# Optimization experiments

Measured on AMD Instinct MI355X. Metric: run time of the kernel, lower is better.

The kernel has to match this reference:

```python
import jax, jax.numpy as jnp
import numpy as np

NEG_INF = -1e9


def setup_inputs() -> dict:
    key = jax.random.key(0)
    ks = jax.random.split(key, 6)
    B, S, E, D = 32, 2048, 1024, 1024
    dec_hidden = jax.random.normal(ks[0], (B, D), dtype=jnp.float32)
    enc_outputs = jax.random.normal(ks[1], (B, S, E), dtype=jnp.float32)
    mask = jax.random.randint(ks[2], (B, S), 0, 2, dtype=jnp.int32)
    # scale weights ~ Glorot-ish so tanh isn't saturated
    W_enc = jax.random.normal(ks[3], (D, E), dtype=jnp.float32) / np.sqrt(E)
    W_dec = jax.random.normal(ks[4], (D, D), dtype=jnp.float32) / np.sqrt(D)
    v = jax.random.normal(ks[5], (D,), dtype=jnp.float32) / np.sqrt(D)
    return {"dec_hidden": dec_hidden, "enc_outputs": enc_outputs, "mask": mask,
            "W_enc": W_enc, "W_dec": W_dec, "v": v}


def reference(dec_hidden, enc_outputs, mask, W_enc, W_dec, v):
    # dh: [B, D]  (torch Linear: x @ W.T)
    dh = dec_hidden @ W_dec.T
    # eh: [B, S, D]
    eh = jnp.einsum('bse,de->bsd', enc_outputs, W_enc)
    # additive energy + projection by v -> scores [B, S]
    energy = jnp.tanh(dh[:, None, :] + eh)
    scores = jnp.einsum('bsd,d->bs', energy, v)
    scores = jnp.where(mask == 0, NEG_INF, scores)
    weights = jax.nn.softmax(scores, axis=1)          # [B, S]
    context = jnp.einsum('bs,bse->be', weights, enc_outputs)  # [B, E]
    return context, weights
```

## Files before the change

### kernel.cpp

```cpp
#include <hip/hip_runtime.h>
#include <stdint.h>

typedef float f32x4 __attribute__((ext_vector_type(4)));
typedef float f32x16 __attribute__((ext_vector_type(16)));
typedef short bf16x8 __attribute__((ext_vector_type(8)));
typedef unsigned short ushort8 __attribute__((ext_vector_type(8)));

__device__ __forceinline__ unsigned short f2bf(float x) {
  union { float f; uint32_t u; } c; c.f = x;
  return (unsigned short)((c.u + 0x8000u) >> 16);
}
__device__ __forceinline__ float bf2f(unsigned short u) {
  union { uint32_t u; float f; } c; c.u = ((uint32_t)u) << 16;
  return c.f;
}


__global__ void prep_fused_k(const float* __restrict__ W, unsigned short* __restrict__ Wt,
                             const float* __restrict__ dec, const float* __restrict__ Wd,
                             float* __restrict__ dh) {
  if (blockIdx.x < 512) {
    int t = blockIdx.x * 256 + threadIdx.x;
    int d  = t >> 7;
    int c0 = (t & 127) << 3;
    const float* src = W + ((size_t)d << 10) + c0;
    f32x4 f0 = *(const f32x4*)src;
    f32x4 f1 = *(const f32x4*)(src + 4);
    ushort8 u;
    u[0]=f2bf(f0[0]); u[1]=f2bf(f0[1]); u[2]=f2bf(f0[2]); u[3]=f2bf(f0[3]);
    u[4]=f2bf(f1[0]); u[5]=f2bf(f1[1]); u[6]=f2bf(f1[2]); u[7]=f2bf(f1[3]);
    int nt = d >> 7, r = d & 127;
    int kt = c0 >> 5, kb = (c0 & 31) >> 3;
    *(ushort8*)(Wt + (((size_t)(nt * 32 + kt)) << 12) + kb * 1024 + r * 8) = u;
  } else {
    __shared__ float sdec[1024];
    int bb = blockIdx.x - 512;
    int b = bb >> 2;
    for (int i = threadIdx.x; i < 1024; i += 256) sdec[i] = dec[(b << 10) + i];
    __syncthreads();
    int d = ((bb & 3) << 8) + threadIdx.x;
    const float* wr = Wd + ((size_t)d << 10);
    float a = 0.f;
    for (int k = 0; k < 1024; k += 4) {
      f32x4 wv = *(const f32x4*)(wr + k);
      f32x4 xv = *(const f32x4*)(&sdec[k]);
      a += wv[0]*xv[0] + wv[1]*xv[1] + wv[2]*xv[2] + wv[3]*xv[3];
    }
    dh[(b << 10) + d] = a;
  }
}

__global__ void compact_k(const int* __restrict__ mask, int* __restrict__ rows,
                          int* __restrict__ cnt, float* __restrict__ wout) {
  int b = blockIdx.x, tid = threadIdx.x;
  int lane = tid & 63, wv = tid >> 6;
  int mloc[8]; int c = 0;
  #pragma unroll
  for (int ii = 0; ii < 8; ++ii) {
    int s = tid * 8 + ii;
    int m = mask[(b << 11) + s];
    mloc[ii] = m; c += m;
    wout[(b << 11) + s] = 0.f;
  }
  int inc = c;
  #pragma unroll
  for (int off = 1; off < 64; off <<= 1) {
    int nn = __shfl_up(inc, off);
    if (lane >= off) inc += nn;
  }
  __shared__ int wsum[4];
  if (lane == 63) wsum[wv] = inc;
  __syncthreads();
  int base = 0;
  for (int w = 0; w < wv; ++w) base += wsum[w];
  int idx = base + inc - c;
  #pragma unroll
  for (int ii = 0; ii < 8; ++ii) {
    if (mloc[ii]) { rows[(b << 11) + idx] = tid * 8 + ii; ++idx; }
  }
  if (tid == 0) cnt[b] = wsum[0] + wsum[1] + wsum[2] + wsum[3];
}

__global__ void pack7_k(const float* __restrict__ enc, const int* __restrict__ rows,
                        const int* __restrict__ cnt, unsigned short* __restrict__ encP) {
  int b = blockIdx.x >> 4, mt = blockIdx.x & 15;
  int n = cnt[b];
  if (mt * 128 >= n) return;
  __shared__ int sr[128];
  if (threadIdx.x < 128) {
    int i = mt * 128 + threadIdx.x; if (i >= n) i = n - 1;
    sr[threadIdx.x] = rows[(b << 11) + i];
  }
  __syncthreads();
  unsigned short* dst = encP + (((size_t)(b * 16 + mt)) << 17);
  for (int it = 0; it < 64; ++it) {
    int idx = it * 256 + threadIdx.x;
    int r   = idx >> 7;
    int c0  = (idx & 127) << 3;
    const float* src = enc + (((size_t)(b << 11) + sr[r]) << 10) + c0;
    f32x4 f0 = *(const f32x4*)src;
    f32x4 f1 = *(const f32x4*)(src + 4);
    ushort8 u;
    u[0]=f2bf(f0[0]); u[1]=f2bf(f0[1]); u[2]=f2bf(f0[2]); u[3]=f2bf(f0[3]);
    u[4]=f2bf(f1[0]); u[5]=f2bf(f1[1]); u[6]=f2bf(f1[2]); u[7]=f2bf(f1[3]);
    int kt = c0 >> 5, kb = (c0 & 31) >> 3;
    *(ushort8*)(dst + (kt << 12) + kb * 1024 + r * 8) = u;
  }
}

__global__ __launch_bounds__(256, 3) void score7_k(
    const unsigned short* __restrict__ encP, const unsigned short* __restrict__ Wt,
    const float* __restrict__ dh, const float* __restrict__ v,
    const int* __restrict__ cnt, float* __restrict__ pscores)
{
  int L  = (blockIdx.x & 7) * 512 + (blockIdx.x >> 3);
  int b  = L >> 7, mt = (L >> 3) & 15, nt = L & 7;
  int n  = cnt[b];
  if (mt * 128 >= n) return;

  __shared__ __align__(16) unsigned short AS[2][4096];
  __shared__ __align__(16) unsigned short BS[2][4096];
  __shared__ float sc[128][2];

  int tid  = threadIdx.x;
  int lane = tid & 63;
  int wv   = tid >> 6;
  int wm = wv >> 1, wn = wv & 1;
  int l31 = lane & 31, l5 = lane >> 5;

  const unsigned short* aT = encP + (((size_t)(b * 16 + mt)) << 17);
  const unsigned short* bT = Wt + (((size_t)nt) << 17);

  int offA[2][2], offB[2][2];
  #pragma unroll
  for (int mf = 0; mf < 2; ++mf) {
    int r = wm * 64 + mf * 32 + l31;
    #pragma unroll
    for (int ki = 0; ki < 2; ++ki)
      offA[mf][ki] = ((ki * 2 + l5) << 10) + r * 8;
  }
  #pragma unroll
  for (int nf = 0; nf < 2; ++nf) {
    int r = wn * 64 + nf * 32 + l31;
    #pragma unroll
    for (int ki = 0; ki < 2; ++ki)
      offB[nf][ki] = ((ki * 2 + l5) << 10) + r * 8;
  }

  f32x16 acc[2][2];
  #pragma unroll
  for (int i = 0; i < 2; ++i)
    #pragma unroll
    for (int j = 0; j < 2; ++j)
      #pragma unroll
      for (int e = 0; e < 16; ++e)
        acc[i][j][e] = 0.f;

  auto stage = [&](int slot, int kt) {
    #pragma unroll
    for (int j = 0; j < 2; ++j) {
      int chunk = wv * 2 + j;
      __builtin_amdgcn_global_load_lds(
        (const __attribute__((address_space(1))) void*)(const void*)(aT + ((size_t)kt << 12) + chunk * 512 + lane * 8),
        (__attribute__((address_space(3))) void*)(void*)(&AS[slot][chunk * 512]), 16, 0, 0);
      __builtin_amdgcn_global_load_lds(
        (const __attribute__((address_space(1))) void*)(const void*)(bT + ((size_t)kt << 12) + chunk * 512 + lane * 8),
        (__attribute__((address_space(3))) void*)(void*)(&BS[slot][chunk * 512]), 16, 0, 0);
    }
  };

  auto compute = [&](int slot) {
    bf16x8 af[2][2], bf[2][2];
    #pragma unroll
    for (int mf = 0; mf < 2; ++mf)
      #pragma unroll
      for (int ki = 0; ki < 2; ++ki)
        af[mf][ki] = *(const bf16x8*)&AS[slot][offA[mf][ki]];
    #pragma unroll
    for (int nf = 0; nf < 2; ++nf)
      #pragma unroll
      for (int ki = 0; ki < 2; ++ki)
        bf[nf][ki] = *(const bf16x8*)&BS[slot][offB[nf][ki]];
    #pragma unroll
    for (int ki = 0; ki < 2; ++ki)
      #pragma unroll
      for (int mf = 0; mf < 2; ++mf)
        #pragma unroll
        for (int nf = 0; nf < 2; ++nf)
          acc[mf][nf] = __builtin_amdgcn_mfma_f32_32x32x16_bf16(af[mf][ki], bf[nf][ki], acc[mf][nf], 0, 0, 0);
  };

  stage(0, 0);
  __syncthreads();
  int slot = 0;
  for (int kt = 0; kt < 31; ++kt) {
    stage(slot ^ 1, kt + 1);
    compute(slot);
    __syncthreads();
    slot ^= 1;
  }
  compute(slot);

  float vv[2], dd[2];
  #pragma unroll
  for (int nf = 0; nf < 2; ++nf) {
    int dcol = nt * 128 + wn * 64 + nf * 32 + l31;
    vv[nf] = v[dcol];
    dd[nf] = dh[(b << 10) + dcol];
  }
  #pragma unroll
  for (int mf = 0; mf < 2; ++mf) {
    #pragma unroll
    for (int reg = 0; reg < 16; ++reg) {
      float p = 0.f;
      #pragma unroll
      for (int nf = 0; nf < 2; ++nf) {
        float x = acc[mf][nf][reg] + dd[nf];
        float e = __expf(2.0f * x);
        float t = 1.0f - __fdividef(2.0f, e + 1.0f);
        p += vv[nf] * t;
      }
      p += __shfl_xor(p, 1); p += __shfl_xor(p, 2); p += __shfl_xor(p, 4);
      p += __shfl_xor(p, 8); p += __shfl_xor(p, 16);
      if (l31 == 0) {
        int row = wm * 64 + mf * 32 + (reg & 3) + 8 * (reg >> 2) + 4 * l5;
        sc[row][wn] = p;
      }
    }
  }
  __syncthreads();
  if (tid < 128) {
    int i = mt * 128 + tid;
    if (i < n)
      pscores[(((size_t)nt) << 16) + (b << 11) + i] = sc[tid][0] + sc[tid][1];
  }
}

__global__ void softmax4_k(const float* __restrict__ ps, const int* __restrict__ rows,
                           const int* __restrict__ cnt, float* __restrict__ wout,
                           float* __restrict__ wc) {
  int b = blockIdx.x;
  int tid = threadIdx.x;
  int n = cnt[b];
  float val[8];
  float m = -INFINITY;
  #pragma unroll
  for (int ii = 0; ii < 8; ++ii) {
    int i = tid + ii * 256;
    float s = -INFINITY;
    if (i < n) {
      s = 0.f;
      #pragma unroll
      for (int nt = 0; nt < 8; ++nt) s += ps[(((size_t)nt) << 16) + (b << 11) + i];
    }
    val[ii] = s;
    m = fmaxf(m, s);
  }
  #pragma unroll
  for (int off = 1; off < 64; off <<= 1) m = fmaxf(m, __shfl_xor(m, off));
  __shared__ float r1[4], r2[4];
  if ((tid & 63) == 0) r1[tid >> 6] = m;
  __syncthreads();
  m = fmaxf(fmaxf(r1[0], r1[1]), fmaxf(r1[2], r1[3]));
  float ssum = 0.f;
  #pragma unroll
  for (int ii = 0; ii < 8; ++ii) { val[ii] = __expf(val[ii] - m); ssum += val[ii]; }
  #pragma unroll
  for (int off = 1; off < 64; off <<= 1) ssum += __shfl_xor(ssum, off);
  if ((tid & 63) == 0) r2[tid >> 6] = ssum;
  __syncthreads();
  ssum = r2[0] + r2[1] + r2[2] + r2[3];
  float inv = 1.0f / ssum;
  #pragma unroll
  for (int ii = 0; ii < 8; ++ii) {
    int i = tid + ii * 256;
    if (i < n) {
      float w = val[ii] * inv;
      wc[(b << 11) + i] = w;
      wout[((size_t)b << 11) + rows[(b << 11) + i]] = w;
    }
  }
}

__global__ void ctx7_k(const unsigned short* __restrict__ encP, const float* __restrict__ wc,
                       const int* __restrict__ cnt, float* __restrict__ cp) {
  int b = blockIdx.x >> 4, mt = blockIdx.x & 15;
  int n = cnt[b];
  float* out = cp + (((size_t)(b * 16 + mt)) << 10);
  int tid = threadIdx.x;
  if (mt * 128 >= n) {
    #pragma unroll
    for (int j = 0; j < 4; ++j) out[tid * 4 + j] = 0.f;
    return;
  }
  __shared__ float sw[128];
  __shared__ float red[128][8];
  if (tid < 128) {
    int i = mt * 128 + tid;
    sw[tid] = (i < n) ? wc[(b << 11) + i] : 0.f;
  }
  __syncthreads();
  const unsigned short* tile = encP + (((size_t)(b * 16 + mt)) << 17);
  int cb8  = tid & 127;
  int half = tid >> 7;
  const unsigned short* base = tile + ((cb8 >> 2) << 12) + ((cb8 & 3) << 10);
  float a[8];
  #pragma unroll
  for (int j = 0; j < 8; ++j) a[j] = 0.f;
  for (int rr = 0; rr < 64; ++rr) {
    int r = half * 64 + rr;
    float w = sw[r];
    ushort8 u = *(const ushort8*)(base + r * 8);
    #pragma unroll
    for (int j = 0; j < 8; ++j) a[j] += w * bf2f(u[j]);
  }
  if (half == 1) {
    #pragma unroll
    for (int j = 0; j < 8; ++j) red[cb8][j] = a[j];
  }
  __syncthreads();
  if (half == 0) {
    int g = cb8 >> 2, kb = cb8 & 3;
    #pragma unroll
    for (int j = 0; j < 8; ++j) out[g * 32 + kb * 8 + j] = a[j] + red[cb8][j];
  }
}

__global__ void ctx_red4_k(const float* __restrict__ cp, float* __restrict__ out) {
  int t = blockIdx.x * 256 + threadIdx.x;
  int b = t >> 10, e = t & 1023;
  float a = 0.f;
  #pragma unroll
  for (int mt = 0; mt < 16; ++mt) a += cp[(((size_t)(b * 16 + mt)) << 10) + e];
  out[t] = a;
}

extern "C" void kernel_launch(void* const* d_in, const int* in_sizes, int n_in,
                              void* d_out, int out_size, void* d_ws, size_t ws_size,
                              hipStream_t stream) {
  const float* dec  = (const float*)d_in[0];
  const float* enc  = (const float*)d_in[1];
  const int*   mask = (const int*)d_in[2];
  const float* Wenc = (const float*)d_in[3];
  const float* Wdec = (const float*)d_in[4];
  const float* v    = (const float*)d_in[5];
  float* out_ctx = (float*)d_out;
  float* out_w   = (float*)d_out + 32768;

  char* ws = (char*)d_ws;
  unsigned short* Wt = (unsigned short*)ws;
  float* dh    = (float*)(ws + (2u << 20));
  int*   rows  = (int*)(ws + (2u << 20) + (128u << 10));
  float* wc    = (float*)(ws + (2u << 20) + (384u << 10));
  int*   cnt   = (int*)(ws + (2u << 20) + (640u << 10));
  float* pscores = (float*)(ws + (3u << 20));
  float* cp      = (float*)(ws + (5u << 20));
  unsigned short* encP = (unsigned short*)(ws + (8ull << 20));

  hipLaunchKernelGGL(prep_fused_k, dim3(640),  dim3(256), 0, stream, Wenc, Wt, dec, Wdec, dh);
  hipLaunchKernelGGL(compact_k,    dim3(32),   dim3(256), 0, stream, mask, rows, cnt, out_w);
  hipLaunchKernelGGL(pack7_k,      dim3(512),  dim3(256), 0, stream, enc, rows, cnt, encP);
  hipLaunchKernelGGL(score7_k,     dim3(4096), dim3(256), 0, stream, encP, Wt, dh, v, cnt, pscores);
  hipLaunchKernelGGL(softmax4_k,   dim3(32),   dim3(256), 0, stream, pscores, rows, cnt, out_w, wc);
  hipLaunchKernelGGL(ctx7_k,       dim3(512),  dim3(256), 0, stream, encP, wc, cnt, cp);
  hipLaunchKernelGGL(ctx_red4_k,   dim3(128),  dim3(256), 0, stream, cp, out_ctx);
}
```

Baseline: 229.6 us.

## Double K-tile depth to 64 and stage pack writes through swizzled LDS

The packed bf16 layout for both the encoder tiles and W_enc moves from 32-wide to 64-wide K blocks. The score GEMM therefore runs 16 K iterations instead of 32, halving barrier count and doubling LDS buffers, with launch bounds lowered from 3 to 2 blocks per CU. The pack kernel now transposes through an XOR-swizzled LDS tile so global writes are fully contiguous. The context kernel is updated to the new layout. The cost is larger LDS use and lower occupancy in the GEMM.

Measured after the change: 242.3 us. +5.5%, slower.

```diff
diff --git a/kernel.cpp b/kernel.cpp
--- a/kernel.cpp
+++ b/kernel.cpp
@@ -30,8 +30,8 @@
     u[0]=f2bf(f0[0]); u[1]=f2bf(f0[1]); u[2]=f2bf(f0[2]); u[3]=f2bf(f0[3]);
     u[4]=f2bf(f1[0]); u[5]=f2bf(f1[1]); u[6]=f2bf(f1[2]); u[7]=f2bf(f1[3]);
     int nt = d >> 7, r = d & 127;
-    int kt = c0 >> 5, kb = (c0 & 31) >> 3;
-    *(ushort8*)(Wt + (((size_t)(nt * 32 + kt)) << 12) + kb * 1024 + r * 8) = u;
+    int kt = c0 >> 6, kb = (c0 & 63) >> 3;
+    *(ushort8*)(Wt + ((size_t)nt << 17) + (kt << 13) + ((kb * 128 + r) << 3)) = u;
   } else {
     __shared__ float sdec[1024];
     int bb = blockIdx.x - 512;
@@ -81,34 +81,47 @@
   if (tid == 0) cnt[b] = wsum[0] + wsum[1] + wsum[2] + wsum[3];
 }
 
-__global__ void pack7_k(const float* __restrict__ enc, const int* __restrict__ rows,
+__global__ void pack8_k(const float* __restrict__ enc, const int* __restrict__ rows,
                         const int* __restrict__ cnt, unsigned short* __restrict__ encP) {
   int b = blockIdx.x >> 4, mt = blockIdx.x & 15;
   int n = cnt[b];
   if (mt * 128 >= n) return;
   __shared__ int sr[128];
-  if (threadIdx.x < 128) {
-    int i = mt * 128 + threadIdx.x; if (i >= n) i = n - 1;
-    sr[threadIdx.x] = rows[(b << 11) + i];
+  __shared__ unsigned short T[128 * 64];
+  int tid = threadIdx.x;
+  if (tid < 128) {
+    int i = mt * 128 + tid; if (i >= n) i = n - 1;
+    sr[tid] = rows[(b << 11) + i];
   }
   __syncthreads();
   unsigned short* dst = encP + (((size_t)(b * 16 + mt)) << 17);
-  for (int it = 0; it < 64; ++it) {
-    int idx = it * 256 + threadIdx.x;
-    int r   = idx >> 7;
-    int c0  = (idx & 127) << 3;
-    const float* src = enc + (((size_t)(b << 11) + sr[r]) << 10) + c0;
-    f32x4 f0 = *(const f32x4*)src;
-    f32x4 f1 = *(const f32x4*)(src + 4);
-    ushort8 u;
-    u[0]=f2bf(f0[0]); u[1]=f2bf(f0[1]); u[2]=f2bf(f0[2]); u[3]=f2bf(f0[3]);
-    u[4]=f2bf(f1[0]); u[5]=f2bf(f1[1]); u[6]=f2bf(f1[2]); u[7]=f2bf(f1[3]);
-    int kt = c0 >> 5, kb = (c0 & 31) >> 3;
-    *(ushort8*)(dst + (kt << 12) + kb * 1024 + r * 8) = u;
-  }
-}
-
-__global__ __launch_bounds__(256, 3) void score7_k(
+  for (int kt = 0; kt < 16; ++kt) {
+    #pragma unroll
+    for (int p = 0; p < 4; ++p) {
+      int id = p * 256 + tid;
+      int r = id >> 3, cseg = id & 7;
+      const float* src = enc + (((size_t)(b << 11) + sr[r]) << 10) + (kt << 6) + (cseg << 3);
+      f32x4 f0 = *(const f32x4*)src;
+      f32x4 f1 = *(const f32x4*)(src + 4);
+      ushort8 u;
+      u[0]=f2bf(f0[0]); u[1]=f2bf(f0[1]); u[2]=f2bf(f0[2]); u[3]=f2bf(f0[3]);
+      u[4]=f2bf(f1[0]); u[5]=f2bf(f1[1]); u[6]=f2bf(f1[2]); u[7]=f2bf(f1[3]);
+      *(ushort8*)&T[(r << 6) + ((cseg ^ (r & 7)) << 3)] = u;
+    }
+    __syncthreads();
+    unsigned short* g = dst + (kt << 13);
+    #pragma unroll
+    for (int p = 0; p < 4; ++p) {
+      int blk = p * 256 + tid;
+      int kb = blk >> 7, r = blk & 127;
+      ushort8 u = *(const ushort8*)&T[(r << 6) + ((kb ^ (r & 7)) << 3)];
+      *(ushort8*)(g + (blk << 3)) = u;
+    }
+    __syncthreads();
+  }
+}
+
+__global__ __launch_bounds__(256, 2) void score8_k(
     const unsigned short* __restrict__ encP, const unsigned short* __restrict__ Wt,
     const float* __restrict__ dh, const float* __restrict__ v,
     const int* __restrict__ cnt, float* __restrict__ pscores)
@@ -118,8 +131,8 @@
   int n  = cnt[b];
   if (mt * 128 >= n) return;
 
-  __shared__ __align__(16) unsigned short AS[2][4096];
-  __shared__ __align__(16) unsigned short BS[2][4096];
+  __shared__ __align__(16) unsigned short AS[2][8192];
+  __shared__ __align__(16) unsigned short BS[2][8192];
   __shared__ float sc[128][2];
 
   int tid  = threadIdx.x;
@@ -129,22 +142,22 @@
   int l31 = lane & 31, l5 = lane >> 5;
 
   const unsigned short* aT = encP + (((size_t)(b * 16 + mt)) << 17);
-  const unsigned short* bT = Wt + (((size_t)nt) << 17);
-
-  int offA[2][2], offB[2][2];
+  const unsigned short* bT = Wt + ((size_t)nt << 17);
+
+  int offA[2][4], offB[2][4];
   #pragma unroll
   for (int mf = 0; mf < 2; ++mf) {
     int r = wm * 64 + mf * 32 + l31;
     #pragma unroll
-    for (int ki = 0; ki < 2; ++ki)
-      offA[mf][ki] = ((ki * 2 + l5) << 10) + r * 8;
+    for (int ki = 0; ki < 4; ++ki)
+      offA[mf][ki] = (((ki * 2 + l5) << 7) + r) << 3;
   }
   #pragma unroll
   for (int nf = 0; nf < 2; ++nf) {
     int r = wn * 64 + nf * 32 + l31;
     #pragma unroll
-    for (int ki = 0; ki < 2; ++ki)
-      offB[nf][ki] = ((ki * 2 + l5) << 10) + r * 8;
+    for (int ki = 0; ki < 4; ++ki)
+      offB[nf][ki] = (((ki * 2 + l5) << 7) + r) << 3;
   }
 
   f32x16 acc[2][2];
@@ -158,42 +171,37 @@
 
   auto stage = [&](int slot, int kt) {
     #pragma unroll
-    for (int j = 0; j < 2; ++j) {
-      int chunk = wv * 2 + j;
+    for (int j = 0; j < 4; ++j) {
+      int off = j * 2048 + tid * 8;
       __builtin_amdgcn_global_load_lds(
-        (const __attribute__((address_space(1))) void*)(const void*)(aT + ((size_t)kt << 12) + chunk * 512 + lane * 8),
-        (__attribute__((address_space(3))) void*)(void*)(&AS[slot][chunk * 512]), 16, 0, 0);
+        (const __attribute__((address_space(1))) void*)(const void*)(aT + ((size_t)kt << 13) + off),
+        (__attribute__((address_space(3))) void*)(void*)(&AS[slot][off]), 16, 0, 0);
       __builtin_amdgcn_global_load_lds(
-        (const __attribute__((address_space(1))) void*)(const void*)(bT + ((size_t)kt << 12) + chunk * 512 + lane * 8),
-        (__attribute__((address_space(3))) void*)(void*)(&BS[slot][chunk * 512]), 16, 0, 0);
+        (const __attribute__((address_space(1))) void*)(const void*)(bT + ((size_t)kt << 13) + off),
+        (__attribute__((address_space(3))) void*)(void*)(&BS[slot][off]), 16, 0, 0);
     }
   };
 
   auto compute = [&](int slot) {
-    bf16x8 af[2][2], bf[2][2];
-    #pragma unroll
-    for (int mf = 0; mf < 2; ++mf)
-      #pragma unroll
-      for (int ki = 0; ki < 2; ++ki)
-        af[mf][ki] = *(const bf16x8*)&AS[slot][offA[mf][ki]];
-    #pragma unroll
-    for (int nf = 0; nf < 2; ++nf)
-      #pragma unroll
-      for (int ki = 0; ki < 2; ++ki)
-        bf[nf][ki] = *(const bf16x8*)&BS[slot][offB[nf][ki]];
-    #pragma unroll
-    for (int ki = 0; ki < 2; ++ki)
+    #pragma unroll
+    for (int ki = 0; ki < 4; ++ki) {
+      bf16x8 af[2], bf[2];
+      #pragma unroll
+      for (int mf = 0; mf < 2; ++mf) af[mf] = *(const bf16x8*)&AS[slot][offA[mf][ki]];
+      #pragma unroll
+      for (int nf = 0; nf < 2; ++nf) bf[nf] = *(const bf16x8*)&BS[slot][offB[nf][ki]];
       #pragma unroll
       for (int mf = 0; mf < 2; ++mf)
         #pragma unroll
         for (int nf = 0; nf < 2; ++nf)
-          acc[mf][nf] = __builtin_amdgcn_mfma_f32_32x32x16_bf16(af[mf][ki], bf[nf][ki], acc[mf][nf], 0, 0, 0);
+          acc[mf][nf] = __builtin_amdgcn_mfma_f32_32x32x16_bf16(af[mf], bf[nf], acc[mf][nf], 0, 0, 0);
+    }
   };
 
   stage(0, 0);
   __syncthreads();
   int slot = 0;
-  for (int kt = 0; kt < 31; ++kt) {
+  for (int kt = 0; kt < 15; ++kt) {
     stage(slot ^ 1, kt + 1);
     compute(slot);
     __syncthreads();
@@ -282,7 +290,7 @@
   }
 }
 
-__global__ void ctx7_k(const unsigned short* __restrict__ encP, const float* __restrict__ wc,
+__global__ void ctx8_k(const unsigned short* __restrict__ encP, const float* __restrict__ wc,
                        const int* __restrict__ cnt, float* __restrict__ cp) {
   int b = blockIdx.x >> 4, mt = blockIdx.x & 15;
   int n = cnt[b];
@@ -303,14 +311,14 @@
   const unsigned short* tile = encP + (((size_t)(b * 16 + mt)) << 17);
   int cb8  = tid & 127;
   int half = tid >> 7;
-  const unsigned short* base = tile + ((cb8 >> 2) << 12) + ((cb8 & 3) << 10);
+  const unsigned short* base = tile + ((cb8 >> 3) << 13) + ((cb8 & 7) << 10);
   float a[8];
   #pragma unroll
   for (int j = 0; j < 8; ++j) a[j] = 0.f;
   for (int rr = 0; rr < 64; ++rr) {
     int r = half * 64 + rr;
     float w = sw[r];
-    ushort8 u = *(const ushort8*)(base + r * 8);
+    ushort8 u = *(const ushort8*)(base + (r << 3));
     #pragma unroll
     for (int j = 0; j < 8; ++j) a[j] += w * bf2f(u[j]);
   }
@@ -320,9 +328,8 @@
   }
   __syncthreads();
   if (half == 0) {
-    int g = cb8 >> 2, kb = cb8 & 3;
-    #pragma unroll
-    for (int j = 0; j < 8; ++j) out[g * 32 + kb * 8 + j] = a[j] + red[cb8][j];
+    #pragma unroll
+    for (int j = 0; j < 8; ++j) out[cb8 * 8 + j] = a[j] + red[cb8][j];
   }
 }
 
@@ -359,9 +366,9 @@
 
   hipLaunchKernelGGL(prep_fused_k, dim3(640),  dim3(256), 0, stream, Wenc, Wt, dec, Wdec, dh);
   hipLaunchKernelGGL(compact_k,    dim3(32),   dim3(256), 0, stream, mask, rows, cnt, out_w);
-  hipLaunchKernelGGL(pack7_k,      dim3(512),  dim3(256), 0, stream, enc, rows, cnt, encP);
-  hipLaunchKernelGGL(score7_k,     dim3(4096), dim3(256), 0, stream, encP, Wt, dh, v, cnt, pscores);
+  hipLaunchKernelGGL(pack8_k,      dim3(512),  dim3(256), 0, stream, enc, rows, cnt, encP);
+  hipLaunchKernelGGL(score8_k,     dim3(4096), dim3(256), 0, stream, encP, Wt, dh, v, cnt, pscores);
   hipLaunchKernelGGL(softmax4_k,   dim3(32),   dim3(256), 0, stream, pscores, rows, cnt, out_w, wc);
-  hipLaunchKernelGGL(ctx7_k,       dim3(512),  dim3(256), 0, stream, encP, wc, cnt, cp);
+  hipLaunchKernelGGL(ctx8_k,       dim3(512),  dim3(256), 0, stream, encP, wc, cnt, cp);
   hipLaunchKernelGGL(ctx_red4_k,   dim3(128),  dim3(256), 0, stream, cp, out_ctx);
 }
```
